# Kernel tuning notes

Hardware: AMD Instinct MI355X
Metric: run time of the kernel (lower is better)

Reference implementation:

```python
import jax, jax.numpy as jnp
import numpy as np

B, H, P, D, NF = 16, 16, 128, 128, 12  # patches == head_dim required by lin_qk


def setup_inputs() -> dict:
    key = jax.random.key(0)
    ks = jax.random.split(key, 8)
    return {
        "q": jax.random.normal(ks[0], (B, H, P, D), jnp.float32),
        "k": jax.random.normal(ks[1], (B, H, P, D), jnp.float32),
        "scale": jnp.ones((1,), jnp.float32),  # unused by the original forward
        "grid": jnp.arange(NF, dtype=jnp.float32) + 1.0,
        "base_weight": jax.random.uniform(ks[2], (D, D), jnp.float32),
        "coef_q": jax.random.uniform(ks[3], (D, NF), jnp.float32),
        "coef_k": jax.random.uniform(ks[4], (D, NF), jnp.float32),
        "scale_base": jnp.ones((1, H, P, D), jnp.float32),
        "scale_sp": jnp.ones((1, H, P, D), jnp.float32),
        "w_qk": jax.random.normal(ks[5], (D, D), jnp.float32) / np.float32(np.sqrt(D)),
        "b_qk": jnp.zeros((D,), jnp.float32),
    }


def _branch(x, coef, grid, base_weight, scale_sp, scale_base):
    # base path: SiLU(x) @ W^T  (F.linear semantics)
    base = jax.nn.silu(x) @ base_weight.T
    # KAN sin basis: sin(grid_f * x_d) -> (B,H,P,NF,D); contract coef[d,f]
    s = jnp.sin(grid[:, None] * x[..., None, :])
    f = jnp.einsum('df,bhpfd->bhpd', coef, s)
    return jax.nn.sigmoid(f * scale_sp + base * scale_base)


def reference(q, k, scale, grid, base_weight, coef_q, coef_k, scale_base, scale_sp, w_qk, b_qk):
    # Per-channel sigmoids, then sum over D. The original builds the full
    # (B,H,P,P,D) broadcast tensor sig_q[...,p,None,:] + sig_k[...,None,p',:]
    # and sums over D; that is exactly separable:
    #   sum_d(sig_q[p,d]) + sum_d(sig_k[p',d])
    sq = _branch(q, coef_q, grid, base_weight, scale_sp, scale_base).sum(-1)  # (B,H,P)
    sk = _branch(k, coef_k, grid, base_weight, scale_sp, scale_base).sum(-1)  # (B,H,P)
    f_out = sq[..., :, None] + sk[..., None, :]  # (B,H,P,P)
    f_out = f_out @ w_qk.T + b_qk  # lin_qk: valid because patches == head_dim
    return jax.nn.softmax(f_out, axis=-1)
```

## Files before the change

### kernel.cpp

```cpp
#include <hip/hip_runtime.h>
#include <hip/hip_bf16.h>


typedef float          f32x4 __attribute__((ext_vector_type(4)));
typedef short          s16x8 __attribute__((ext_vector_type(8)));
typedef int            s32x4 __attribute__((ext_vector_type(4)));
typedef unsigned short u16x8 __attribute__((ext_vector_type(8)));

#define LOG2E   1.44269504f
#define NLOG2E -1.44269504f
#define INV2PI  0.15915494309189535f

static __device__ __forceinline__ float hw_exp2(float x) {
    float r;
    asm("v_exp_f32 %0, %1" : "=v"(r) : "v"(x));
    return r;
}
static __device__ __forceinline__ float hw_fract(float x) {
    float r;
    asm("v_fract_f32 %0, %1" : "=v"(r) : "v"(x));
    return r;
}
static __device__ __forceinline__ float hw_sin01(float f) {
    float r;
    asm("v_sin_f32 %0, %1" : "=v"(r) : "v"(f));
    return r;
}
static __device__ __forceinline__ float hw_cos01(float f) {
    float r;
    asm("v_cos_f32 %0, %1" : "=v"(r) : "v"(f));
    return r;
}
static __device__ __forceinline__ float fastrcp(float x) {
    return __builtin_amdgcn_rcpf(x);
}
static __device__ __forceinline__ unsigned int cvt_pk_bf16(float lo, float hi) {
    unsigned int r;
    asm("v_cvt_pk_bf16_f32 %0, %1, %2" : "=v"(r) : "v"(lo), "v"(hi));
    return r;
}
static __device__ __forceinline__ float sigmoid_fast(float z) {
    return fastrcp(1.f + hw_exp2(z * NLOG2E));
}
static __device__ __forceinline__ int swz(int local) {
    return local ^ (((local >> 8) & 7) << 4);
}

__global__ __launch_bounds__(256) void k_convert(const float* __restrict__ bw,
                                                 unsigned short* __restrict__ wbf) {
    int i = blockIdx.x * 256 + threadIdx.x;
    if (i < 128 * 128) {
        __hip_bfloat16 h = __float2bfloat16(bw[i]);
        unsigned short r;
        __builtin_memcpy(&r, &h, 2);
        wbf[i] = r;
    }
}

__global__ __launch_bounds__(512, 4) void k_branch(
    const float* __restrict__ q, const float* __restrict__ k,
    const unsigned short* __restrict__ wbf,
    const float* __restrict__ gridv,
    const float* __restrict__ coef_q, const float* __restrict__ coef_k,
    const float* __restrict__ sbase,
    const float* __restrict__ ssp,
    float* __restrict__ sums_lo, float* __restrict__ sums_hi)
{
    __shared__ char smem[32768 + 6144];
    float* cfl = (float*)(smem + 32768);

    const int t = threadIdx.x;
    const int lane = t & 63, w = t >> 6;
    const int wr = w >> 1;
    const int ch = w & 1;
    const int r15 = lane & 15, g4 = lane >> 4;
    const int row0 = blockIdx.x * 64;
    const bool is_q = row0 < 32768;
    const float* X = is_q ? q : k;
    const float* coef = is_q ? coef_q : coef_k;
    const int xrow0 = is_q ? row0 : row0 - 32768;
    const float g1 = gridv[0];
    const float grev = g1 * INV2PI;

    #pragma unroll
    for (int it = 0; it < 4; ++it) {
        int c = it * 512 + t;
        u16x8 v = *(const u16x8*)&wbf[c * 8];
        *(u16x8*)(smem + swz(c * 16)) = v;
    }
    #pragma unroll
    for (int it = 0; it < 3; ++it) {
        int e = it * 512 + t;
        float v = coef[e];
        int d = e / 12, u = e - d * 12;
        cfl[u * 128 + d] = v;
    }
    __syncthreads();

    const int xrow = wr * 16 + r15;
    const float* xrowp = &X[(xrow0 + xrow) * 128];
    const int hp = (row0 + xrow) & 2047;
    const float* ssprow = &ssp[hp * 128];

    f32x4 acc[4];
    #pragma unroll
    for (int n = 0; n < 4; ++n) acc[n] = (f32x4){0.f, 0.f, 0.f, 0.f};
    float fv[16];

    #pragma unroll
    for (int s = 0; s < 4; ++s) {
        const float4* xp = (const float4*)&xrowp[s * 32 + g4 * 8];
        float4 x0 = xp[0], x1 = xp[1];
        float xsv[8] = {x0.x, x0.y, x0.z, x0.w, x1.x, x1.y, x1.z, x1.w};
        float sl[8];
        #pragma unroll
        for (int j = 0; j < 8; ++j) {
            float e = hw_exp2(xsv[j] * NLOG2E);
            sl[j] = xsv[j] * fastrcp(1.f + e);
        }
        s32x4 a4 = {(int)cvt_pk_bf16(sl[0], sl[1]), (int)cvt_pk_bf16(sl[2], sl[3]),
                    (int)cvt_pk_bf16(sl[4], sl[5]), (int)cvt_pk_bf16(sl[6], sl[7])};
        s16x8 af = __builtin_bit_cast(s16x8, a4);

        if ((s >> 1) == ch) {
            const int s2 = s & 1;
            const float4* spp = (const float4*)&ssprow[s * 32 + g4 * 8];
            float4 sp0 = spp[0], sp1 = spp[1];
            float spv[8] = {sp0.x, sp0.y, sp0.z, sp0.w,
                            sp1.x, sp1.y, sp1.z, sp1.w};
            #pragma unroll
            for (int j = 0; j < 8; ++j) {
                int d = s * 32 + g4 * 8 + j;
                float rev = hw_fract(grev * xsv[j]);
                float s1 = hw_sin01(rev);
                float cv = hw_cos01(rev);
                float t2 = cv + cv;
                float sprev = 0.f, scur = s1;
                float f = cfl[d] * s1;
                #pragma unroll
                for (int u = 1; u < 12; ++u) {
                    float sn = __builtin_fmaf(t2, scur, -sprev);
                    f = __builtin_fmaf(cfl[u * 128 + d], sn, f);
                    sprev = scur; scur = sn;
                }
                fv[s2 * 8 + j] = f * spv[j];
            }
        }

        #pragma unroll
        for (int n = 0; n < 4; ++n) {
            s16x8 bfw = *(const s16x8*)(smem + swz((ch * 64 + n * 16 + r15) * 256
                                                   + s * 64 + g4 * 16));
            acc[n] = __builtin_amdgcn_mfma_f32_16x16x32_bf16(bfw, af, acc[n], 0, 0, 0);
        }
    }
    __syncthreads();

    float* myfv = (float*)smem + w * 1024;
    #pragma unroll
    for (int s2 = 0; s2 < 2; ++s2) {
        #pragma unroll
        for (int jb = 0; jb < 2; ++jb) {
            int dloc = s2 * 32 + g4 * 8 + jb * 4;
            f32x4 v = {fv[s2*8 + jb*4 + 0], fv[s2*8 + jb*4 + 1],
                       fv[s2*8 + jb*4 + 2], fv[s2*8 + jb*4 + 3]};
            *(f32x4*)&myfv[r15 * 64 + ((dloc + r15 * 4) & 63)] = v;
        }
    }

    float ps = 0.f;
    #pragma unroll
    for (int n = 0; n < 4; ++n) {
        f32x4 fp = *(f32x4*)&myfv[r15 * 64 + ((n * 16 + g4 * 4 + r15 * 4) & 63)];
        float4 sb = *(const float4*)&sbase[hp * 128 + ch * 64 + n * 16 + g4 * 4];
        float sbv[4] = {sb.x, sb.y, sb.z, sb.w};
        #pragma unroll
        for (int reg = 0; reg < 4; ++reg) {
            float z = fp[reg] + acc[n][reg] * sbv[reg];
            ps += sigmoid_fast(z);
        }
    }
    ps += __shfl_xor(ps, 16, 64);
    ps += __shfl_xor(ps, 32, 64);
    if (g4 == 0) {
        (ch ? sums_hi : sums_lo)[row0 + xrow] = ps;
    }
}

__global__ __launch_bounds__(256) void k_attn(
    const float* __restrict__ sums_lo, const float* __restrict__ sums_hi,
    const float* __restrict__ w_qk, const float* __restrict__ b_qk,
    float* __restrict__ out)
{
    __shared__ float skl[128], Tp[2][128], Rp[2][128], Tl[128], Rl[128];
    const int bh = blockIdx.x >> 1;
    const int half = blockIdx.x & 1;
    const int t = threadIdx.x;

    if (t < 128) {
        int idx = 32768 + bh * 128 + t;
        skl[t] = sums_lo[idx] + sums_hi[idx];
    }
    __syncthreads();
    {
        int j = t & 127, ph = t >> 7;
        const float4* wr = (const float4*)&w_qk[j * 128 + ph * 64];
        const float* sk2 = &skl[ph * 64];
        float a = 0.f, r = 0.f;
        #pragma unroll 8
        for (int p4 = 0; p4 < 16; ++p4) {
            float4 w4 = wr[p4];
            a += w4.x * sk2[p4 * 4 + 0] + w4.y * sk2[p4 * 4 + 1] +
                 w4.z * sk2[p4 * 4 + 2] + w4.w * sk2[p4 * 4 + 3];
            r += w4.x + w4.y + w4.z + w4.w;
        }
        Tp[ph][j] = a;
        Rp[ph][j] = r;
    }
    __syncthreads();
    if (t < 128) {
        Tl[t] = Tp[0][t] + Tp[1][t] + b_qk[t];
        Rl[t] = Rp[0][t] + Rp[1][t];
    }
    __syncthreads();

    const int lane = t & 63, w = t >> 6;
    #pragma unroll
    for (int it = 0; it < 16; ++it) {
        int row = bh * 128 + half * 64 + it * 4 + w;
        float sqv = sums_lo[row] + sums_hi[row];
        float2 r2 = *(const float2*)&Rl[lane * 2];
        float2 t2 = *(const float2*)&Tl[lane * 2];
        float l0 = __builtin_fmaf(sqv, r2.x, t2.x);
        float l1 = __builtin_fmaf(sqv, r2.y, t2.y);
        float m = fmaxf(l0, l1);
        #pragma unroll
        for (int s = 32; s >= 1; s >>= 1) m = fmaxf(m, __shfl_xor(m, s, 64));
        float e0 = hw_exp2((l0 - m) * LOG2E);
        float e1 = hw_exp2((l1 - m) * LOG2E);
        float sum = e0 + e1;
        #pragma unroll
        for (int w2 = 32; w2 >= 1; w2 >>= 1) sum += __shfl_xor(sum, w2, 64);
        float inv = fastrcp(sum);
        float2 o2 = {e0 * inv, e1 * inv};
        *(float2*)&out[row * 128 + lane * 2] = o2;
    }
}

extern "C" void kernel_launch(void* const* d_in, const int* in_sizes, int n_in,
                              void* d_out, int out_size, void* d_ws, size_t ws_size,
                              hipStream_t stream) {
    (void)in_sizes; (void)n_in; (void)out_size; (void)ws_size;
    const float* q      = (const float*)d_in[0];
    const float* k      = (const float*)d_in[1];
    const float* gridv  = (const float*)d_in[3];
    const float* bw     = (const float*)d_in[4];
    const float* coef_q = (const float*)d_in[5];
    const float* coef_k = (const float*)d_in[6];
    const float* sbase  = (const float*)d_in[7];
    const float* ssp    = (const float*)d_in[8];
    const float* w_qk   = (const float*)d_in[9];
    const float* b_qk   = (const float*)d_in[10];

    float* out  = (float*)d_out;
    float* ws      = (float*)d_ws;
    float* sums_lo = ws;
    float* sums_hi = ws + 65536;
    unsigned short* wbf = (unsigned short*)(ws + 131072);

    k_convert<<<64, 256, 0, stream>>>(bw, wbf);
    k_branch<<<1024, 512, 0, stream>>>(q, k, wbf, gridv, coef_q, coef_k,
                                       sbase, ssp, sums_lo, sums_hi);
    k_attn<<<512, 256, 0, stream>>>(sums_lo, sums_hi, w_qk, b_qk, out);
}
```

Measured before the change: 41.05 us.

## Remap sin-basis work to per-lane column ownership with coefficients in registers

The KAN sin-basis evaluation is redistributed so each lane owns four fixed output columns across four rows. The 12 coefficients for those columns are held in registers instead of being staged through a transposed shared-memory table, which removes one sync phase and 6 KB of LDS. x and scale_sp are now reloaded from global memory in column-major slices, and the store into the LDS transpose buffer is reindexed to match. The attention kernel also halves its grid so each block handles a full 128-row head, trading parallelism for less duplicated T/R precomputation.

```diff
diff --git a/kernel.cpp b/kernel.cpp
--- a/kernel.cpp
+++ b/kernel.cpp
@@ -66,14 +66,15 @@
     const float* __restrict__ ssp,
     float* __restrict__ sums_lo, float* __restrict__ sums_hi)
 {
-    __shared__ char smem[32768 + 6144];
-    float* cfl = (float*)(smem + 32768);
+    __shared__ char smem[32768];
 
     const int t = threadIdx.x;
     const int lane = t & 63, w = t >> 6;
     const int wr = w >> 1;
     const int ch = w & 1;
     const int r15 = lane & 15, g4 = lane >> 4;
+    const int ce = lane & 15;
+    const int re = lane >> 4;
     const int row0 = blockIdx.x * 64;
     const bool is_q = row0 < 32768;
     const float* X = is_q ? q : k;
@@ -88,19 +89,22 @@
         u16x8 v = *(const u16x8*)&wbf[c * 8];
         *(u16x8*)(smem + swz(c * 16)) = v;
     }
-    #pragma unroll
-    for (int it = 0; it < 3; ++it) {
-        int e = it * 512 + t;
-        float v = coef[e];
-        int d = e / 12, u = e - d * 12;
-        cfl[u * 128 + d] = v;
-    }
-    __syncthreads();
+    __syncthreads();
+
+    const int gcol = ch * 64 + ce * 4;
+    float cf[4][12];
+    #pragma unroll
+    for (int j = 0; j < 4; ++j) {
+        const float4* cp = (const float4*)&coef[(gcol + j) * 12];
+        float4 c0 = cp[0], c1 = cp[1], c2 = cp[2];
+        cf[j][0] = c0.x; cf[j][1] = c0.y; cf[j][2]  = c0.z; cf[j][3]  = c0.w;
+        cf[j][4] = c1.x; cf[j][5] = c1.y; cf[j][6]  = c1.z; cf[j][7]  = c1.w;
+        cf[j][8] = c2.x; cf[j][9] = c2.y; cf[j][10] = c2.z; cf[j][11] = c2.w;
+    }
 
     const int xrow = wr * 16 + r15;
     const float* xrowp = &X[(xrow0 + xrow) * 128];
     const int hp = (row0 + xrow) & 2047;
-    const float* ssprow = &ssp[hp * 128];
 
     f32x4 acc[4];
     #pragma unroll
@@ -122,28 +126,28 @@
                     (int)cvt_pk_bf16(sl[4], sl[5]), (int)cvt_pk_bf16(sl[6], sl[7])};
         s16x8 af = __builtin_bit_cast(s16x8, a4);
 
-        if ((s >> 1) == ch) {
-            const int s2 = s & 1;
-            const float4* spp = (const float4*)&ssprow[s * 32 + g4 * 8];
-            float4 sp0 = spp[0], sp1 = spp[1];
-            float spv[8] = {sp0.x, sp0.y, sp0.z, sp0.w,
-                            sp1.x, sp1.y, sp1.z, sp1.w};
+        {
+            int srow = wr * 16 + re * 4 + s;
+            int shp = (row0 + srow) & 2047;
+            float4 xs4 = *(const float4*)&X[(xrow0 + srow) * 128 + gcol];
+            float4 sp4 = *(const float4*)&ssp[shp * 128 + gcol];
+            float xq[4]  = {xs4.x, xs4.y, xs4.z, xs4.w};
+            float spq[4] = {sp4.x, sp4.y, sp4.z, sp4.w};
             #pragma unroll
-            for (int j = 0; j < 8; ++j) {
-                int d = s * 32 + g4 * 8 + j;
-                float rev = hw_fract(grev * xsv[j]);
+            for (int j = 0; j < 4; ++j) {
+                float rev = hw_fract(grev * xq[j]);
                 float s1 = hw_sin01(rev);
                 float cv = hw_cos01(rev);
                 float t2 = cv + cv;
                 float sprev = 0.f, scur = s1;
-                float f = cfl[d] * s1;
+                float f = cf[j][0] * s1;
                 #pragma unroll
                 for (int u = 1; u < 12; ++u) {
                     float sn = __builtin_fmaf(t2, scur, -sprev);
-                    f = __builtin_fmaf(cfl[u * 128 + d], sn, f);
+                    f = __builtin_fmaf(cf[j][u], sn, f);
                     sprev = scur; scur = sn;
                 }
-                fv[s2 * 8 + j] = f * spv[j];
+                fv[s * 4 + j] = f * spq[j];
             }
         }
 
@@ -158,14 +162,10 @@
 
     float* myfv = (float*)smem + w * 1024;
     #pragma unroll
-    for (int s2 = 0; s2 < 2; ++s2) {
-        #pragma unroll
-        for (int jb = 0; jb < 2; ++jb) {
-            int dloc = s2 * 32 + g4 * 8 + jb * 4;
-            f32x4 v = {fv[s2*8 + jb*4 + 0], fv[s2*8 + jb*4 + 1],
-                       fv[s2*8 + jb*4 + 2], fv[s2*8 + jb*4 + 3]};
-            *(f32x4*)&myfv[r15 * 64 + ((dloc + r15 * 4) & 63)] = v;
-        }
+    for (int s = 0; s < 4; ++s) {
+        int rloc = re * 4 + s;
+        f32x4 v = {fv[s*4+0], fv[s*4+1], fv[s*4+2], fv[s*4+3]};
+        *(f32x4*)&myfv[rloc * 64 + ((ce * 4 + rloc * 4) & 63)] = v;
     }
 
     float ps = 0.f;
@@ -193,8 +193,7 @@
     float* __restrict__ out)
 {
     __shared__ float skl[128], Tp[2][128], Rp[2][128], Tl[128], Rl[128];
-    const int bh = blockIdx.x >> 1;
-    const int half = blockIdx.x & 1;
+    const int bh = blockIdx.x;
     const int t = threadIdx.x;
 
     if (t < 128) {
@@ -225,9 +224,9 @@
     __syncthreads();
 
     const int lane = t & 63, w = t >> 6;
-    #pragma unroll
-    for (int it = 0; it < 16; ++it) {
-        int row = bh * 128 + half * 64 + it * 4 + w;
+    #pragma unroll 8
+    for (int it = 0; it < 32; ++it) {
+        int row = bh * 128 + it * 4 + w;
         float sqv = sums_lo[row] + sums_hi[row];
         float2 r2 = *(const float2*)&Rl[lane * 2];
         float2 t2 = *(const float2*)&Tl[lane * 2];
@@ -271,5 +270,5 @@
     k_convert<<<64, 256, 0, stream>>>(bw, wbf);
     k_branch<<<1024, 512, 0, stream>>>(q, k, wbf, gridv, coef_q, coef_k,
                                        sbase, ssp, sums_lo, sums_hi);
-    k_attn<<<512, 256, 0, stream>>>(sums_lo, sums_hi, w_qk, b_qk, out);
-}
+    k_attn<<<256, 256, 0, stream>>>(sums_lo, sums_hi, w_qk, b_qk, out);
+}
```

After: 45.30 us. 10.4% more time.
